# Performance work log

Measured on AMD Instinct MI355X. Metric: run time of the kernel, lower is better.

## Reference

```python
import jax, jax.numpy as jnp
from jax import lax
import numpy as np

C = 256; NH = 8; NP = 4; FFN = 512; B = 2; H = 128; W = 128
HD = C // NH


def _ln(x, g, b):
    m = jnp.mean(x, -1, keepdims=True)
    v = jnp.var(x, -1, keepdims=True)
    return (x - m) * lax.rsqrt(v + 1e-5) * g + b


def _deform_attn(q, kv, off_w, off_b, attw_w, attw_b, vp_w, vp_b, op_w, op_b):
    # q, kv: (B, N, C) with N = H*W
    Bn, N, Cc = q.shape
    val = (kv @ vp_w + vp_b).reshape(Bn, N, NH, HD)
    off = (q @ off_w + off_b).reshape(Bn, N, NH, NP, 2)
    attw = jax.nn.softmax((q @ attw_w + attw_b).reshape(Bn, N, NH, NP), axis=-1)
    # identity-grid reference points (normalized, pixel centers)
    ry = (jnp.arange(H, dtype=q.dtype) + 0.5) / H
    rx = (jnp.arange(W, dtype=q.dtype) + 0.5) / W
    gy, gx = jnp.meshgrid(ry, rx, indexing='ij')
    ref = jnp.stack([gx.ravel(), gy.ravel()], -1)  # (N, 2) as (x, y)
    norm = jnp.array([W, H], dtype=q.dtype)
    loc = ref[None, :, None, None, :] + off / norm  # (B,N,NH,NP,2) in [0,1]
    # grid_sample align_corners=False, zeros padding
    x = loc[..., 0] * W - 0.5
    y = loc[..., 1] * H - 0.5
    x0 = jnp.floor(x); y0 = jnp.floor(y)
    lx = x - x0; ly = y - y0
    x0i = x0.astype(jnp.int32); y0i = y0.astype(jnp.int32)
    v_t = val.transpose(0, 2, 1, 3)  # (B, NH, N, HD)

    def gather(xi, yi, w):
        valid = (xi >= 0) & (xi < W) & (yi >= 0) & (yi < H)
        idx = jnp.clip(yi, 0, H - 1) * W + jnp.clip(xi, 0, W - 1)  # (B,N,NH,NP)
        idx_t = idx.transpose(0, 2, 1, 3).reshape(Bn, NH, N * NP)
        g = jnp.take_along_axis(v_t, idx_t[..., None], axis=2)
        g = g.reshape(Bn, NH, N, NP, HD)
        wm = (w * valid).transpose(0, 2, 1, 3)  # (B,NH,N,NP)
        return g * wm[..., None]

    samp = (gather(x0i, y0i, (1 - lx) * (1 - ly))
            + gather(x0i + 1, y0i, lx * (1 - ly))
            + gather(x0i, y0i + 1, (1 - lx) * ly)
            + gather(x0i + 1, y0i + 1, lx * ly))  # (B,NH,N,NP,HD)
    out = jnp.einsum('bhnpd,bnhp->bnhd', samp, attw).reshape(Bn, N, Cc)
    return out @ op_w + op_b


def _forward(cam_bev, sat_bev,
             c2s_off_w, c2s_off_b, c2s_attw_w, c2s_attw_b, c2s_vp_w, c2s_vp_b, c2s_op_w, c2s_op_b,
             s2c_off_w, s2c_off_b, s2c_attw_w, s2c_attw_b, s2c_vp_w, s2c_vp_b, s2c_op_w, s2c_op_b,
             ln1_g, ln1_b, ln2_g, ln2_b, lnf_g, lnf_b,
             ffn1_w, ffn1_b, ffn2_w, ffn2_b,
             g1_w, bn_g, bn_b, g2_w, g2_b):
    Bn, Cc, Hh, Ww = cam_bev.shape
    q_cam = cam_bev.reshape(Bn, Cc, Hh * Ww).transpose(0, 2, 1)
    q_sat = sat_bev.reshape(Bn, Cc, Hh * Ww).transpose(0, 2, 1)
    c2s = _deform_attn(q_cam, q_sat, c2s_off_w, c2s_off_b, c2s_attw_w, c2s_attw_b,
                       c2s_vp_w, c2s_vp_b, c2s_op_w, c2s_op_b)
    cam_att = _ln(q_cam + c2s, ln1_g, ln1_b)
    s2c = _deform_attn(q_sat, q_cam, s2c_off_w, s2c_off_b, s2c_attw_w, s2c_attw_b,
                       s2c_vp_w, s2c_vp_b, s2c_op_w, s2c_op_b)
    sat_att = _ln(q_sat + s2c, ln2_g, ln2_b)
    cam_map = cam_att.transpose(0, 2, 1).reshape(Bn, Cc, Hh, Ww)
    sat_map = sat_att.transpose(0, 2, 1).reshape(Bn, Cc, Hh, Ww)
    gi = jnp.concatenate([cam_map, sat_map], axis=1)
    h = lax.conv_general_dilated(gi, g1_w, (1, 1), 'SAME',
                                 dimension_numbers=('NCHW', 'OIHW', 'NCHW'))
    # BatchNorm2d in eval mode: running_mean=0, running_var=1
    h = jax.nn.relu(h * lax.rsqrt(jnp.float32(1.0 + 1e-5)) * bn_g[None, :, None, None]
                    + bn_b[None, :, None, None])
    g = jax.nn.sigmoid(jnp.einsum('bchw,oc->bohw', h, g2_w) + g2_b[None, :, None, None])
    fused = g * cam_map + (1 - g) * sat_map
    ff = fused.reshape(Bn, Cc, Hh * Ww).transpose(0, 2, 1)
    ff = ff + (jax.nn.relu(ff @ ffn1_w + ffn1_b) @ ffn2_w + ffn2_b)
    ff = _ln(ff, lnf_g, lnf_b)
    return ff.transpose(0, 2, 1).reshape(Bn, Cc, Hh, Ww) + cam_bev


def setup_inputs() -> dict:
    key = jax.random.key(0)
    ks = iter(jax.random.split(key, 40))

    def rn(shape, s=0.02):
        return jax.random.normal(next(ks), shape, jnp.float32) * s

    # directional offset-bias init (as in original init_weights)
    thetas = np.arange(NH) * (2.0 * np.pi / NH)
    grid = np.stack([np.cos(thetas), np.sin(thetas)], -1)
    grid = grid / np.abs(grid).max(-1, keepdims=True)
    grid = np.tile(grid[:, None, :], (1, NP, 1)) * np.arange(1, NP + 1)[None, :, None]
    off_bias = jnp.asarray(grid.reshape(-1), jnp.float32)

    def attn_params():
        return dict(off_w=rn((C, NH * NP * 2), 0.01), off_b=off_bias,
                    attw_w=rn((C, NH * NP), 0.02), attw_b=rn((NH * NP,), 0.02),
                    vp_w=rn((C, C), 0.05), vp_b=jnp.zeros((C,), jnp.float32),
                    op_w=rn((C, C), 0.05), op_b=jnp.zeros((C,), jnp.float32))

    p1 = attn_params(); p2 = attn_params()
    inp = {
        'cam_bev': jax.random.normal(next(ks), (B, C, H, W), jnp.float32),
        'sat_bev': jax.random.normal(next(ks), (B, C, H, W), jnp.float32),
    }
    for pre, p in (('c2s_', p1), ('s2c_', p2)):
        for k, v in p.items():
            inp[pre + k] = v
    inp.update(
        ln1_g=jnp.ones((C,), jnp.float32), ln1_b=jnp.zeros((C,), jnp.float32),
        ln2_g=jnp.ones((C,), jnp.float32), ln2_b=jnp.zeros((C,), jnp.float32),
        lnf_g=jnp.ones((C,), jnp.float32), lnf_b=jnp.zeros((C,), jnp.float32),
        ffn1_w=rn((C, FFN), 0.05), ffn1_b=jnp.zeros((FFN,), jnp.float32),
        ffn2_w=rn((FFN, C), 0.05), ffn2_b=jnp.zeros((C,), jnp.float32),
        g1_w=rn((C // 2, 2 * C, 3, 3), 0.02),
        bn_g=jnp.ones((C // 2,), jnp.float32), bn_b=jnp.zeros((C // 2,), jnp.float32),
        g2_w=rn((C, C // 2), 0.02), g2_b=jnp.zeros((C,), jnp.float32),
    )
    return inp


def reference(cam_bev, sat_bev,
              c2s_off_w, c2s_off_b, c2s_attw_w, c2s_attw_b, c2s_vp_w, c2s_vp_b, c2s_op_w, c2s_op_b,
              s2c_off_w, s2c_off_b, s2c_attw_w, s2c_attw_b, s2c_vp_w, s2c_vp_b, s2c_op_w, s2c_op_b,
              ln1_g, ln1_b, ln2_g, ln2_b, lnf_g, lnf_b,
              ffn1_w, ffn1_b, ffn2_w, ffn2_b,
              g1_w, bn_g, bn_b, g2_w, g2_b):
    return _forward(cam_bev, sat_bev,
                    c2s_off_w, c2s_off_b, c2s_attw_w, c2s_attw_b, c2s_vp_w, c2s_vp_b, c2s_op_w, c2s_op_b,
                    s2c_off_w, s2c_off_b, s2c_attw_w, s2c_attw_b, s2c_vp_w, s2c_vp_b, s2c_op_w, s2c_op_b,
                    ln1_g, ln1_b, ln2_g, ln2_b, lnf_g, lnf_b,
                    ffn1_w, ffn1_b, ffn2_w, ffn2_b,
                    g1_w, bn_g, bn_b, g2_w, g2_b)
```

## Files before the change

### kernel.cpp

```cpp
#include <hip/hip_runtime.h>
#include <hip/hip_bf16.h>
#include <cstddef>

#define BBn  2
#define CCn  256
#define HHn  128
#define WWn  128
#define NNn  (HHn*WWn)
#define MTOT (BBn*NNn)
#define PADW 130

typedef unsigned short u16;
typedef __attribute__((ext_vector_type(8))) short bf8v;
typedef __attribute__((ext_vector_type(8))) unsigned short u16x8;
typedef __attribute__((ext_vector_type(4))) float f4v;

typedef __attribute__((address_space(1))) const void gvoid_t;
typedef __attribute__((address_space(3))) void svoid_t;
#define ASYNC16(g, l) __builtin_amdgcn_global_load_lds((gvoid_t*)(g), (svoid_t*)(l), 16, 0, 0)

__device__ __forceinline__ u16 f2bf(float f) {
    __hip_bfloat16 h = __float2bfloat16(f);
    return *reinterpret_cast<u16*>(&h);
}
__device__ __forceinline__ float bf2f(u16 h) {
    return __uint_as_float(((unsigned)h) << 16);
}

struct ZOff {
    long a, w, bia, f1, f2, b1, r, p;
    int ch;
};

template<int BM, int BN, int WC, int EPI, int KK>
__global__ __launch_bounds__(256)
void mgemm(const u16* __restrict__ A, const u16* __restrict__ Wt,
           const float* __restrict__ bias, int ldw, int Nc,
           float* __restrict__ outf, float* __restrict__ outf2,
           u16* __restrict__ outb, const u16* __restrict__ img,
           const void* __restrict__ resid,
           const float* __restrict__ p0, const float* __restrict__ p1,
           int choff, ZOff zo)
{
    constexpr int WR = 4 / WC;
    constexpr int MROWS = BM / WR;
    constexpr int MI = MROWS / 16;
    constexpr int AT = BM / 64;
    constexpr int BT = BN / 64;
    constexpr int NSTEPS = KK / 32;

    __shared__ __align__(16) u16 As[2 * BM * 32];
    __shared__ __align__(16) u16 Bs[2 * BN * 32];
    __shared__ float red[4][64][2];

    const int z = blockIdx.z;
    if (z) {
        A += (long)z * zo.a; Wt += (long)z * zo.w;
        if (bias)  bias  += (long)z * zo.bia;
        if (outf)  outf  += (long)z * zo.f1;
        if (outf2) outf2 += (long)z * zo.f2;
        if (outb)  outb  += (long)z * zo.b1;
        if (p0)    p0    += (long)z * zo.p;
        if (p1)    p1    += (long)z * zo.p;
        choff += z * zo.ch;
    }

    const int tid  = threadIdx.x;
    const int lane = tid & 63;
    const int w    = tid >> 6;
    const int wr   = w / WC, wc = w % WC;
    const int by = blockIdx.y;
    const int m0 = by * BM;
    const int n0 = blockIdx.x * BN;
    const int lr = lane & 15, lq = lane >> 4;

    const u16* gA[AT]; int loA[AT];
    #pragma unroll
    for (int t = 0; t < AT; ++t) {
        int c = t * 256 + tid; int row = c >> 2; int part = c & 3;
        int pg = part ^ ((row >> 1) & 3);
        gA[t] = A + (size_t)(m0 + row) * KK + pg * 8;
        loA[t] = c * 8;
    }
    const u16* gB[BT]; int loB[BT];
    #pragma unroll
    for (int t = 0; t < BT; ++t) {
        int c = t * 256 + tid; int row = c >> 2; int part = c & 3;
        int pg = part ^ ((row >> 1) & 3);
        gB[t] = Wt + (size_t)(n0 + row) * ldw + pg * 8;
        loB[t] = c * 8;
    }

    f4v acc[MI][4];
    if constexpr (EPI == 7 || EPI == 9) {
        const u16* r16 = (const u16*)resid + (EPI == 7 ? (long)z * zo.r : 0);
        #pragma unroll
        for (int j = 0; j < 4; ++j) {
            int n = wc * 64 + j * 16 + lr;
            float bj = bias[n];
            #pragma unroll
            for (int i = 0; i < MI; ++i)
                #pragma unroll
                for (int r = 0; r < 4; ++r) {
                    int m = m0 + i * 16 + lq * 4 + r;
                    acc[i][j][r] = bf2f(r16[(size_t)m * 256 + n]) + bj;
                }
        }
    } else {
        #pragma unroll
        for (int i = 0; i < MI; ++i)
            #pragma unroll
            for (int j = 0; j < 4; ++j)
                acc[i][j] = (f4v){0.f, 0.f, 0.f, 0.f};
    }

    auto stageG = [&](int s, int buf) {
        int k0 = s * 32;
        #pragma unroll
        for (int t = 0; t < AT; ++t)
            ASYNC16(gA[t] + k0, (u16*)As + buf * (BM * 32) + loA[t]);
        #pragma unroll
        for (int t = 0; t < BT; ++t)
            ASYNC16(gB[t] + k0, (u16*)Bs + buf * (BN * 32) + loB[t]);
    };
    auto computeStep = [&](int s) {
        const u16* Ab = As + (s & 1) * (BM * 32);
        const u16* Bb = Bs + (s & 1) * (BN * 32);
        bf8v af[MI], bv[4];
        #pragma unroll
        for (int i = 0; i < MI; ++i) {
            int row = wr * MROWS + i * 16 + lr;
            af[i] = *(const bf8v*)&Ab[row * 32 + ((lq ^ ((row >> 1) & 3)) << 3)];
        }
        #pragma unroll
        for (int j = 0; j < 4; ++j) {
            int row = wc * 64 + j * 16 + lr;
            bv[j] = *(const bf8v*)&Bb[row * 32 + ((lq ^ ((row >> 1) & 3)) << 3)];
        }
        #pragma unroll
        for (int i = 0; i < MI; ++i)
            #pragma unroll
            for (int j = 0; j < 4; ++j)
                acc[i][j] = __builtin_amdgcn_mfma_f32_16x16x32_bf16(af[i], bv[j], acc[i][j], 0, 0, 0);
    };

    stageG(0, 0);
    __syncthreads();
    for (int s = 0; s < NSTEPS - 1; ++s) {
        stageG(s + 1, (s + 1) & 1);
        computeStep(s);
        __syncthreads();
    }
    computeStep(NSTEPS - 1);

    if constexpr (EPI == 7 || EPI == 9) {
        float g4[4], b4[4];
        #pragma unroll
        for (int j = 0; j < 4; ++j) {
            int n = wc * 64 + j * 16 + lr;
            g4[j] = p0[n]; b4[j] = p1[n];
        }
        #pragma unroll
        for (int i = 0; i < MI; ++i)
            #pragma unroll
            for (int r = 0; r < 4; ++r) {
                float p = 0.f, p2 = 0.f;
                #pragma unroll
                for (int j = 0; j < 4; ++j) { float v = acc[i][j][r]; p += v; p2 += v * v; }
                p += __shfl_xor(p, 1, 16);  p2 += __shfl_xor(p2, 1, 16);
                p += __shfl_xor(p, 2, 16);  p2 += __shfl_xor(p2, 2, 16);
                p += __shfl_xor(p, 4, 16);  p2 += __shfl_xor(p2, 4, 16);
                p += __shfl_xor(p, 8, 16);  p2 += __shfl_xor(p2, 8, 16);
                if (lr == 0) {
                    int row = i * 16 + lq * 4 + r;
                    red[w][row][0] = p; red[w][row][1] = p2;
                }
            }
        __syncthreads();
        #pragma unroll
        for (int i = 0; i < MI; ++i) {
            float mean4[4], rstd4[4];
            #pragma unroll
            for (int r = 0; r < 4; ++r) {
                int row = i * 16 + lq * 4 + r;
                float s  = red[0][row][0] + red[1][row][0] + red[2][row][0] + red[3][row][0];
                float s2 = red[0][row][1] + red[1][row][1] + red[2][row][1] + red[3][row][1];
                float mean = s * (1.f / 256.f);
                float var  = s2 * (1.f / 256.f) - mean * mean;
                mean4[r] = mean;
                rstd4[r] = rsqrtf(var + 1e-5f);
            }
            if constexpr (EPI == 7) {
                #pragma unroll
                for (int r = 0; r < 4; ++r) {
                    int m = m0 + i * 16 + lq * 4 + r;
                    int b = m >> 14, sp = m & (NNn - 1);
                    size_t pb = (((size_t)b * PADW + (sp >> 7) + 1) * PADW + (sp & 127) + 1) * 512 + choff;
                    #pragma unroll
                    for (int j = 0; j < 4; ++j) {
                        int n = wc * 64 + j * 16 + lr;
                        outb[pb + n] = f2bf((acc[i][j][r] - mean4[r]) * rstd4[r] * g4[j] + b4[j]);
                    }
                }
            } else {
                int mb = m0 + i * 16 + lq * 4;
                int b = mb >> 14, sp = mb & (NNn - 1);
                #pragma unroll
                for (int j = 0; j < 4; ++j) {
                    int n = wc * 64 + j * 16 + lr;
                    size_t oi = ((size_t)b * 256 + n) * NNn + sp;
                    float4 cv = *(const float4*)&outf2[oi];
                    float4 o;
                    o.x = (acc[i][j][0] - mean4[0]) * rstd4[0] * g4[j] + b4[j] + cv.x;
                    o.y = (acc[i][j][1] - mean4[1]) * rstd4[1] * g4[j] + b4[j] + cv.y;
                    o.z = (acc[i][j][2] - mean4[2]) * rstd4[2] * g4[j] + b4[j] + cv.z;
                    o.w = (acc[i][j][3] - mean4[3]) * rstd4[3] * g4[j] + b4[j] + cv.w;
                    *(float4*)&outf[oi] = o;
                }
            }
        }
        return;
    }

    float bj[4]; int ncol[4];
    #pragma unroll
    for (int j = 0; j < 4; ++j) {
        int n = n0 + wc * 64 + j * 16 + lr;
        ncol[j] = n;
        if constexpr (EPI == 0 || EPI == 4 || EPI == 5) bj[j] = bias[n];
    }
    #pragma unroll
    for (int i = 0; i < MI; ++i) {
        #pragma unroll
        for (int r = 0; r < 4; ++r) {
            int m = m0 + wr * MROWS + i * 16 + lq * 4 + r;
            size_t pb = 0;
            if constexpr (EPI == 4) {
                int b = m >> 14, sp = m & (NNn - 1);
                pb = (((size_t)b * PADW + (sp >> 7) + 1) * PADW + (sp & 127) + 1) * 512;
            }
            #pragma unroll
            for (int j = 0; j < 4; ++j) {
                int n = ncol[j];
                float v = acc[i][j][r];
                size_t oi = (size_t)m * Nc + n;
                if constexpr (EPI == 0) {
                    outb[oi] = f2bf(v + bj[j]);
                } else if constexpr (EPI == 2) {
                    if (n < 64)      outf [(size_t)m * 64 + n]        = v + p0[n];
                    else if (n < 96) outf2[(size_t)m * 32 + (n - 64)] = v + p1[n - 64];
                } else if constexpr (EPI == 4) {
                    float vv = v + bj[j];
                    float g = 1.f / (1.f + __expf(-vv));
                    float f = g * bf2f(img[pb + n]) + (1.f - g) * bf2f(img[pb + 256 + n]);
                    outb[oi] = f2bf(f);
                } else if constexpr (EPI == 5) {
                    outb[oi] = f2bf(fmaxf(v + bj[j], 0.f));
                }
            }
        }
    }
}

template<int TAPS>
__global__ __launch_bounds__(256)
void conv_k(const u16* __restrict__ img, const u16* __restrict__ Wt,
            u16* __restrict__ outp)
{
    constexpr int NS = TAPS * 16;
    __shared__ __align__(16) u16 As[2 * 128 * 32];
    __shared__ __align__(16) u16 Bs[2 * 128 * 32];

    const int z = blockIdx.z;
    outp += (size_t)z * MTOT * 128;
    const int tid = threadIdx.x;
    const int lane = tid & 63;
    const int w = tid >> 6;
    const int wr = w >> 1, wc = w & 1;
    int by = blockIdx.y;
    by = ((by & 7) << 5) | (by >> 3);
    const int m0 = by * 128;
    const int lr = lane & 15, lq = lane >> 4;

    const u16* abase[2]; const u16* bbase[2]; int ldsOff[2];
    #pragma unroll
    for (int t = 0; t < 2; ++t) {
        int c = t * 256 + tid;
        int row = c >> 2, part = c & 3;
        int pg = part ^ ((row >> 1) & 3);
        ldsOff[t] = c * 8;
        int m = m0 + row; int b = m >> 14; int sp = m & (NNn - 1);
        long cb = ((long)b * PADW + (sp >> 7)) * PADW + (sp & 127);
        abase[t] = img + cb * 512 + pg * 8;
        bbase[t] = Wt + (size_t)row * 4608 + pg * 8;
    }

    long adel[TAPS]; int bdel[TAPS];
    #pragma unroll
    for (int tt = 0; tt < TAPS; ++tt) {
        int tap = z * TAPS + tt;
        int dy = tap / 3, dx = tap - dy * 3;
        adel[tt] = (long)(dy * PADW + dx) * 512;
        bdel[tt] = tap * 512;
    }

    f4v acc[4][4];
    #pragma unroll
    for (int i = 0; i < 4; ++i)
        #pragma unroll
        for (int j = 0; j < 4; ++j)
            acc[i][j] = (f4v){0.f, 0.f, 0.f, 0.f};

    auto stage = [&](int s, int buf) {
        int tt = s >> 4;
        int ci = (s & 15) * 32;
        #pragma unroll
        for (int t = 0; t < 2; ++t) {
            ASYNC16(abase[t] + adel[tt] + ci, (u16*)As + buf * (128 * 32) + ldsOff[t]);
            ASYNC16(bbase[t] + bdel[tt] + ci, (u16*)Bs + buf * (128 * 32) + ldsOff[t]);
        }
    };
    auto computeStep = [&](int s) {
        const u16* Ab = As + (s & 1) * (128 * 32);
        const u16* Bb = Bs + (s & 1) * (128 * 32);
        bf8v af[4], bv[4];
        #pragma unroll
        for (int i = 0; i < 4; ++i) {
            int row = wr * 64 + i * 16 + lr;
            af[i] = *(const bf8v*)&Ab[row * 32 + ((lq ^ ((row >> 1) & 3)) << 3)];
        }
        #pragma unroll
        for (int j = 0; j < 4; ++j) {
            int row = wc * 64 + j * 16 + lr;
            bv[j] = *(const bf8v*)&Bb[row * 32 + ((lq ^ ((row >> 1) & 3)) << 3)];
        }
        #pragma unroll
        for (int i = 0; i < 4; ++i)
            #pragma unroll
            for (int j = 0; j < 4; ++j)
                acc[i][j] = __builtin_amdgcn_mfma_f32_16x16x32_bf16(af[i], bv[j], acc[i][j], 0, 0, 0);
    };

    stage(0, 0);
    __syncthreads();
    #pragma unroll 4
    for (int s = 0; s < NS - 1; ++s) {
        stage(s + 1, (s + 1) & 1);
        computeStep(s);
        __syncthreads();
    }
    computeStep(NS - 1);

    #pragma unroll
    for (int i = 0; i < 4; ++i)
        #pragma unroll
        for (int r = 0; r < 4; ++r) {
            int m = m0 + wr * 64 + i * 16 + lq * 4 + r;
            #pragma unroll
            for (int j = 0; j < 4; ++j) {
                int n = wc * 64 + j * 16 + lr;
                outp[(size_t)m * 128 + n] = f2bf(acc[i][j][r]);
            }
        }
}

__global__ __launch_bounds__(256)
void combine_k(const u16* __restrict__ part, const float* __restrict__ bng,
               const float* __restrict__ bnb, u16* __restrict__ hb)
{
    const float bnscale = rsqrtf(1.0f + 1e-5f);
    int i = (blockIdx.x * 256 + threadIdx.x) * 4;
    int n = i & 127;
    float s0 = 0.f, s1 = 0.f, s2 = 0.f, s3 = 0.f;
    #pragma unroll
    for (int p = 0; p < 3; ++p) {
        ushort4 a = *(const ushort4*)&part[(size_t)p * MTOT * 128 + i];
        s0 += bf2f(a.x); s1 += bf2f(a.y); s2 += bf2f(a.z); s3 += bf2f(a.w);
    }
    ushort4 o;
    o.x = f2bf(fmaxf(s0 * bnscale * bng[n + 0] + bnb[n + 0], 0.f));
    o.y = f2bf(fmaxf(s1 * bnscale * bng[n + 1] + bnb[n + 1], 0.f));
    o.z = f2bf(fmaxf(s2 * bnscale * bng[n + 2] + bnb[n + 2], 0.f));
    o.w = f2bf(fmaxf(s3 * bnscale * bng[n + 3] + bnb[n + 3], 0.f));
    *(ushort4*)&hb[i] = o;
}

__global__ __launch_bounds__(256)
void zring_k(u16* __restrict__ pad)
{
    int i = blockIdx.x * 256 + threadIdx.x;
    if (i >= 66048) return;
    int e = i * 8;
    const int per_b = 264192;
    int b = e / per_b; int r = e - b * per_b;
    long off;
    if (r < 66560)       { int x = r >> 9, c = r & 511;                 off = (((long)b * PADW + 0)   * PADW + x)   * 512 + c; }
    else if (r < 133120) { int r2 = r - 66560;  int x = r2 >> 9, c = r2 & 511; off = (((long)b * PADW + 129) * PADW + x)   * 512 + c; }
    else if (r < 198656) { int r2 = r - 133120; int y = (r2 >> 9) + 1, c = r2 & 511; off = (((long)b * PADW + y)   * PADW + 0)   * 512 + c; }
    else                 { int r2 = r - 198656; int y = (r2 >> 9) + 1, c = r2 & 511; off = (((long)b * PADW + y)   * PADW + 129) * 512 + c; }
    *(u16x8*)(pad + off) = (u16x8){0, 0, 0, 0, 0, 0, 0, 0};
}

__global__ __launch_bounds__(256)
void tcvt_k(const float* __restrict__ cam, const float* __restrict__ sat,
            u16* __restrict__ qcam, u16* __restrict__ qsat)
{
    __shared__ float t[64][65];
    int z = blockIdx.z;
    const float* src = (z < 2) ? cam : sat;
    u16* dst = (z < 2) ? qcam : qsat;
    int b = z & 1;
    int c0 = blockIdx.x * 64, sp0 = blockIdx.y * 64;
    #pragma unroll
    for (int it = 0; it < 16; ++it) {
        int idx = it * 256 + threadIdx.x;
        int cl = idx >> 6, sl = idx & 63;
        t[cl][sl] = src[((size_t)(b * CCn + c0 + cl)) * NNn + sp0 + sl];
    }
    __syncthreads();
    #pragma unroll
    for (int it = 0; it < 16; ++it) {
        int idx = it * 256 + threadIdx.x;
        int sl = idx >> 6, cl = idx & 63;
        dst[((size_t)(b * NNn + sp0 + sl)) * CCn + c0 + cl] = f2bf(t[cl][sl]);
    }
}

__global__ __launch_bounds__(256)
void sample_k(const u16* __restrict__ val, const float* __restrict__ off,
              const float* __restrict__ lg, u16* __restrict__ outp)
{
    __shared__ uint2 desc[64][17];

    int z = blockIdx.z;
    val  += (size_t)z * MTOT * CCn;
    off  += (size_t)z * MTOT * 64;
    lg   += (size_t)z * MTOT * 32;
    outp += (size_t)z * MTOT * CCn;

    const int tid = threadIdx.x;
    const int rh0 = blockIdx.x * 64;

    if (tid < 64) {
        int rhg = rh0 + tid;
        int h = rhg & 7, rn = rhg >> 3;
        int n = rn & (NNn - 1), b = rn >> 14;
        int yp = n >> 7, xp = n & 127;

        const float* ofp = off + (size_t)rn * 64 + h * 8;
        const float* lgp = lg  + (size_t)rn * 32 + h * 4;
        float4 of0 = *(const float4*)ofp;
        float4 of1 = *(const float4*)(ofp + 4);
        float4 lgv = *(const float4*)lgp;
        float ofx[4] = { of0.x, of0.z, of1.x, of1.z };
        float ofy[4] = { of0.y, of0.w, of1.y, of1.w };

        float mx = fmaxf(fmaxf(lgv.x, lgv.y), fmaxf(lgv.z, lgv.w));
        float e0 = __expf(lgv.x - mx), e1 = __expf(lgv.y - mx);
        float e2 = __expf(lgv.z - mx), e3 = __expf(lgv.w - mx);
        float inv = 1.f / (e0 + e1 + e2 + e3);
        float aw[4] = { e0 * inv, e1 * inv, e2 * inv, e3 * inv };

        unsigned hb = (unsigned)(b * NNn) * 256u + h * 32;
        #pragma unroll
        for (int p = 0; p < 4; ++p) {
            float xs = (float)xp + ofx[p];
            float ys = (float)yp + ofy[p];
            float x0f = floorf(xs), y0f = floorf(ys);
            float lx = xs - x0f, ly = ys - y0f;
            int x0 = (int)x0f, y0 = (int)y0f;
            #pragma unroll
            for (int c = 0; c < 4; ++c) {
                int xi = x0 + (c & 1), yi = y0 + (c >> 1);
                bool valid = (xi >= 0) & (xi < WWn) & (yi >= 0) & (yi < HHn);
                float wgt = valid
                    ? aw[p] * ((c & 1) ? lx : 1.f - lx) * ((c >> 1) ? ly : 1.f - ly)
                    : 0.f;
                int xc = min(max(xi, 0), WWn - 1);
                int yc = min(max(yi, 0), HHn - 1);
                unsigned addr = hb + (unsigned)(yc * WWn + xc) * 256u;
                desc[tid][p * 4 + c] = make_uint2(addr, __float_as_uint(wgt));
            }
        }
    }
    __syncthreads();

    const int rh = tid >> 2;
    const int q  = tid & 3;
    const int rhg = rh0 + rh;
    const int h = rhg & 7, rn = rhg >> 3;

    float a[8];
    #pragma unroll
    for (int e = 0; e < 8; ++e) a[e] = 0.f;
    #pragma unroll
    for (int k = 0; k < 16; ++k) {
        uint2 d = desc[rh][k];
        float wgt = __uint_as_float(d.y);
        u16x8 v = *(const u16x8*)(val + d.x + q * 8);
        #pragma unroll
        for (int e = 0; e < 8; ++e)
            a[e] += wgt * bf2f(v[e]);
    }
    u16x8 o;
    #pragma unroll
    for (int e = 0; e < 8; ++e) o[e] = f2bf(a[e]);
    *(u16x8*)(outp + (size_t)rn * CCn + h * 32 + q * 8) = o;
}

__global__ __launch_bounds__(256)
void repack_all(const float* __restrict__ vp1, const float* __restrict__ op1,
                const float* __restrict__ vp2, const float* __restrict__ op2,
                const float* __restrict__ f1w, const float* __restrict__ f2w,
                const float* __restrict__ of1, const float* __restrict__ aw1,
                const float* __restrict__ of2, const float* __restrict__ aw2,
                const float* __restrict__ g1,  const float* __restrict__ g2,
                const float* __restrict__ vpb1, const float* __restrict__ vpb2,
                const float* __restrict__ opb1, const float* __restrict__ opb2,
                const float* __restrict__ ofb1, const float* __restrict__ awb1,
                const float* __restrict__ ofb2, const float* __restrict__ awb2,
                const float* __restrict__ l1g, const float* __restrict__ l1b,
                const float* __restrict__ l2g, const float* __restrict__ l2b,
                u16* __restrict__ wb, float* __restrict__ bb)
{
    int i = blockIdx.x * 256 + threadIdx.x;
    if (i >= 1212416 + 2240) return;
    if (i >= 1212416) {
        int j = i - 1212416;
        float v;
        if      (j < 256)  v = vpb1[j];
        else if (j < 512)  v = vpb2[j - 256];
        else if (j < 768)  v = opb1[j - 512];
        else if (j < 1024) v = opb2[j - 768];
        else if (j < 1088) v = ofb1[j - 1024];
        else if (j < 1120) v = awb1[j - 1088];
        else if (j < 1184) v = ofb2[j - 1120];
        else if (j < 1216) v = awb2[j - 1184];
        else if (j < 1472) v = l1g[j - 1216];
        else if (j < 1728) v = l1b[j - 1472];
        else if (j < 1984) v = l2g[j - 1728];
        else               v = l2b[j - 1984];
        bb[j] = v;
        return;
    }
    float v;
    if (i < 262144) {
        const float* src[4] = { vp1, vp2, op1, op2 };
        int q = i >> 16, j = i & 65535;
        int n = j >> 8, k = j & 255;
        v = src[q][(size_t)k * 256 + n];
    } else if (i < 393216) {
        int j = i - 262144; int n = j >> 8, k = j & 255;
        v = f1w[(size_t)k * 512 + n];
    } else if (i < 524288) {
        int j = i - 393216; int n = j >> 9, k = j & 511;
        v = f2w[(size_t)k * 256 + n];
    } else if (i < 589824) {
        int jj = i - 524288; int hh = jj >> 15; int j = jj & 32767;
        int n = j >> 8, k = j & 255;
        const float* ofw = hh ? of2 : of1;
        const float* aww = hh ? aw2 : aw1;
        if (n < 64)      v = ofw[(size_t)k * 64 + n];
        else if (n < 96) v = aww[(size_t)k * 32 + (n - 64)];
        else             v = 0.f;
    } else if (i < 1179648) {
        int j = i - 589824; int co = j / 4608, k = j - co * 4608;
        int tap = k >> 9, ci = k & 511;
        v = g1[((size_t)co * 512 + ci) * 9 + tap];
    } else {
        int j = i - 1179648; int n = j >> 7, k = j & 127;
        v = g2[(size_t)n * 128 + k];
    }
    wb[i] = f2bf(v);
}

extern "C" void kernel_launch(void* const* d_in, const int* in_sizes, int n_in,
                              void* d_out, int out_size, void* d_ws, size_t ws_size,
                              hipStream_t stream)
{
    const float* cam_bev   = (const float*)d_in[0];
    const float* sat_bev   = (const float*)d_in[1];
    const float* c2s_off_w  = (const float*)d_in[2];
    const float* c2s_off_b  = (const float*)d_in[3];
    const float* c2s_attw_w = (const float*)d_in[4];
    const float* c2s_attw_b = (const float*)d_in[5];
    const float* c2s_vp_w   = (const float*)d_in[6];
    const float* c2s_vp_b   = (const float*)d_in[7];
    const float* c2s_op_w   = (const float*)d_in[8];
    const float* c2s_op_b   = (const float*)d_in[9];
    const float* s2c_off_w  = (const float*)d_in[10];
    const float* s2c_off_b  = (const float*)d_in[11];
    const float* s2c_attw_w = (const float*)d_in[12];
    const float* s2c_attw_b = (const float*)d_in[13];
    const float* s2c_vp_w   = (const float*)d_in[14];
    const float* s2c_vp_b   = (const float*)d_in[15];
    const float* s2c_op_w   = (const float*)d_in[16];
    const float* s2c_op_b   = (const float*)d_in[17];
    const float* ln1_g = (const float*)d_in[18];
    const float* ln1_b = (const float*)d_in[19];
    const float* ln2_g = (const float*)d_in[20];
    const float* ln2_b = (const float*)d_in[21];
    const float* lnf_g = (const float*)d_in[22];
    const float* lnf_b = (const float*)d_in[23];
    const float* ffn1_w = (const float*)d_in[24];
    const float* ffn1_b = (const float*)d_in[25];
    const float* ffn2_w = (const float*)d_in[26];
    const float* ffn2_b = (const float*)d_in[27];
    const float* g1_w  = (const float*)d_in[28];
    const float* bn_g  = (const float*)d_in[29];
    const float* bn_b  = (const float*)d_in[30];
    const float* g2_w  = (const float*)d_in[31];
    const float* g2_b  = (const float*)d_in[32];

    char* base = (char*)d_ws;
    size_t off = 0;
    auto alloc = [&](size_t bytes) -> void* {
        void* p = base + off;
        off += (bytes + 255) & ~(size_t)255;
        return p;
    };

    u16*   qcam   = (u16*)  alloc((size_t)MTOT * CCn * 2 * 2);
    u16*   qsat   = qcam + (size_t)MTOT * CCn;
    u16*   valb   = (u16*)  alloc((size_t)MTOT * CCn * 2 * 2);
    u16*   sampb  = (u16*)  alloc((size_t)MTOT * CCn * 2 * 2);
    float* offb   = (float*)alloc((size_t)MTOT * 64 * 4 * 2);
    float* attwb  = (float*)alloc((size_t)MTOT * 32 * 4 * 2);
    size_t padBytes = (size_t)BBn * PADW * PADW * 512 * 2;
    u16*   pad    = (u16*)  alloc(padBytes);
    u16*   hbuf   = (u16*)  alloc((size_t)MTOT * 128 * 2);
    u16*   convpart = (u16*)alloc((size_t)3 * MTOT * 128 * 2);
    u16*   wbase  = (u16*)  alloc((size_t)1212416 * 2);
    float* biasbf = (float*)alloc((size_t)2240 * 4);
    u16* wvp = wbase;
    u16* wop = wbase + 131072;
    u16* wf1 = wbase + 262144;
    u16* wf2 = wbase + 393216;
    u16* woa = wbase + 524288;
    u16* wcv = wbase + 589824;
    u16* wg2 = wbase + 1179648;
    u16*   fused_bf = valb;
    u16*   midb     = qcam;

    dim3 blk(256);
    ZOff zz{0, 0, 0, 0, 0, 0, 0, 0, 0};

    zring_k<<<258, blk, 0, stream>>>(pad);
    tcvt_k<<<dim3(4, 256, 4), blk, 0, stream>>>(cam_bev, sat_bev, qcam, qsat);
    repack_all<<<4746, blk, 0, stream>>>(c2s_vp_w, c2s_op_w, s2c_vp_w, s2c_op_w,
                                         ffn1_w, ffn2_w, c2s_off_w, c2s_attw_w,
                                         s2c_off_w, s2c_attw_w, g1_w, g2_w,
                                         c2s_vp_b, s2c_vp_b, c2s_op_b, s2c_op_b,
                                         c2s_off_b, c2s_attw_b, s2c_off_b, s2c_attw_b,
                                         ln1_g, ln1_b, ln2_g, ln2_b,
                                         wbase, biasbf);

    {
        ZOff zo{ -(long)MTOT * CCn, 65536, 256, 0, 0, (long)MTOT * CCn, 0, 0, 0 };
        mgemm<128, 128, 2, 0, 256><<<dim3(2, 256, 2), blk, 0, stream>>>(
            qsat, wvp, biasbf, 256, 256,
            nullptr, nullptr, valb, nullptr, nullptr, nullptr, nullptr, 0, zo);
    }
    {
        ZOff zo{ (long)MTOT * CCn, 32768, 0, (long)MTOT * 64, (long)MTOT * 32, 0, 0, 96, 0 };
        mgemm<64, 128, 2, 2, 256><<<dim3(1, 512, 2), blk, 0, stream>>>(
            qcam, woa, nullptr, 256, 128,
            offb, attwb, nullptr, nullptr, nullptr, biasbf + 1024, biasbf + 1088, 0, zo);
    }
    sample_k<<<dim3(4096, 1, 2), blk, 0, stream>>>(valb, offb, attwb, sampb);
    {
        ZOff zo{ (long)MTOT * CCn, 65536, 256, 0, 0, 0, (long)MTOT * CCn, 512, 256 };
        mgemm<64, 256, 4, 7, 256><<<dim3(1, 512, 2), blk, 0, stream>>>(
            sampb, wop, biasbf + 512, 256, 256,
            nullptr, nullptr, pad, nullptr, qcam, biasbf + 1216, biasbf + 1472, 0, zo);
    }
    conv_k<3><<<dim3(1, 256, 3), blk, 0, stream>>>(pad, wcv, convpart);
    combine_k<<<4096, blk, 0, stream>>>(convpart, bn_g, bn_b, hbuf);

    mgemm<64, 128, 2, 4, 128><<<dim3(2, 512, 1), blk, 0, stream>>>(
        hbuf, wg2, g2_b, 128, 256,
        nullptr, nullptr, fused_bf, pad, nullptr, nullptr, nullptr, 0, zz);

    mgemm<128, 128, 2, 5, 256><<<dim3(4, 256, 1), blk, 0, stream>>>(
        fused_bf, wf1, ffn1_b, 256, 512,
        nullptr, nullptr, midb, nullptr, nullptr, nullptr, nullptr, 0, zz);
    mgemm<64, 256, 4, 9, 512><<<dim3(1, 512, 1), blk, 0, stream>>>(
        midb, wf2, ffn2_b, 512, 256,
        (float*)d_out, (float*)cam_bev, nullptr, nullptr, fused_bf, lnf_g, lnf_b, 0, zz);
}
```

Before: 279.7 us.

## Merge prologue kernels and fuse value-proj with offset/attn GEMM into one launch

Combines the ring-zeroing, input transpose/convert and weight repack kernels into a single prologue launch, and merges the value-projection GEMM and the offset/attention-logit GEMM into one kernel that dispatches blocks by job. The aim is to cut launch count and the tail bubbles between small dependent kernels, letting the two independent GEMMs share the GPU concurrently. The combined GEMM computes all 128 columns for the offset job, where the old config used a narrower tile. Block-level branching may also lower occupancy uniformity.

```diff
diff --git a/kernel.cpp b/kernel.cpp
--- a/kernel.cpp
+++ b/kernel.cpp
@@ -227,7 +227,7 @@
     for (int j = 0; j < 4; ++j) {
         int n = n0 + wc * 64 + j * 16 + lr;
         ncol[j] = n;
-        if constexpr (EPI == 0 || EPI == 4 || EPI == 5) bj[j] = bias[n];
+        if constexpr (EPI == 4 || EPI == 5) bj[j] = bias[n];
     }
     #pragma unroll
     for (int i = 0; i < MI; ++i) {
@@ -244,12 +244,7 @@
                 int n = ncol[j];
                 float v = acc[i][j][r];
                 size_t oi = (size_t)m * Nc + n;
-                if constexpr (EPI == 0) {
-                    outb[oi] = f2bf(v + bj[j]);
-                } else if constexpr (EPI == 2) {
-                    if (n < 64)      outf [(size_t)m * 64 + n]        = v + p0[n];
-                    else if (n < 96) outf2[(size_t)m * 32 + (n - 64)] = v + p1[n - 64];
-                } else if constexpr (EPI == 4) {
+                if constexpr (EPI == 4) {
                     float vv = v + bj[j];
                     float g = 1.f / (1.f + __expf(-vv));
                     float f = g * bf2f(img[pb + n]) + (1.f - g) * bf2f(img[pb + 256 + n]);
@@ -259,6 +254,126 @@
                 }
             }
         }
+    }
+}
+
+__global__ __launch_bounds__(256)
+void vpoa_k(const u16* __restrict__ qcam, const u16* __restrict__ wvp,
+            const u16* __restrict__ woa, const float* __restrict__ biasbf,
+            u16* __restrict__ valb, float* __restrict__ offb,
+            float* __restrict__ attwb)
+{
+    __shared__ __align__(16) u16 As[2 * 128 * 32];
+    __shared__ __align__(16) u16 Bs[2 * 128 * 32];
+
+    const int bx = blockIdx.x;
+    int job, zs, by, n0;
+    if (bx < 1024) { job = 0; zs = bx >> 9; int r = bx & 511; n0 = (r & 1) * 128; by = r >> 1; }
+    else           { job = 1; int r = bx - 1024; zs = r >> 8; by = r & 255; n0 = 0; }
+
+    const u16* A  = job == 0 ? qcam + (size_t)(1 - zs) * MTOT * CCn
+                             : qcam + (size_t)zs * MTOT * CCn;
+    const u16* Wt = job == 0 ? wvp + zs * 65536 : woa + zs * 32768;
+
+    const int tid  = threadIdx.x;
+    const int lane = tid & 63;
+    const int w    = tid >> 6;
+    const int wr   = w >> 1, wc = w & 1;
+    const int m0 = by * 128;
+    const int lr = lane & 15, lq = lane >> 4;
+
+    const u16* gA[2]; int loA[2];
+    const u16* gB[2]; int loB[2];
+    #pragma unroll
+    for (int t = 0; t < 2; ++t) {
+        int c = t * 256 + tid; int row = c >> 2; int part = c & 3;
+        int pg = part ^ ((row >> 1) & 3);
+        gA[t] = A + (size_t)(m0 + row) * 256 + pg * 8;
+        gB[t] = Wt + (size_t)(n0 + row) * 256 + pg * 8;
+        loA[t] = c * 8; loB[t] = c * 8;
+    }
+
+    f4v acc[4][4];
+    #pragma unroll
+    for (int i = 0; i < 4; ++i)
+        #pragma unroll
+        for (int j = 0; j < 4; ++j)
+            acc[i][j] = (f4v){0.f, 0.f, 0.f, 0.f};
+
+    auto stageG = [&](int s, int buf) {
+        int k0 = s * 32;
+        #pragma unroll
+        for (int t = 0; t < 2; ++t) {
+            ASYNC16(gA[t] + k0, (u16*)As + buf * (128 * 32) + loA[t]);
+            ASYNC16(gB[t] + k0, (u16*)Bs + buf * (128 * 32) + loB[t]);
+        }
+    };
+    auto computeStep = [&](int s) {
+        const u16* Ab = As + (s & 1) * (128 * 32);
+        const u16* Bb = Bs + (s & 1) * (128 * 32);
+        bf8v af[4], bv[4];
+        #pragma unroll
+        for (int i = 0; i < 4; ++i) {
+            int row = wr * 64 + i * 16 + lr;
+            af[i] = *(const bf8v*)&Ab[row * 32 + ((lq ^ ((row >> 1) & 3)) << 3)];
+        }
+        #pragma unroll
+        for (int j = 0; j < 4; ++j) {
+            int row = wc * 64 + j * 16 + lr;
+            bv[j] = *(const bf8v*)&Bb[row * 32 + ((lq ^ ((row >> 1) & 3)) << 3)];
+        }
+        #pragma unroll
+        for (int i = 0; i < 4; ++i)
+            #pragma unroll
+            for (int j = 0; j < 4; ++j)
+                acc[i][j] = __builtin_amdgcn_mfma_f32_16x16x32_bf16(af[i], bv[j], acc[i][j], 0, 0, 0);
+    };
+
+    stageG(0, 0);
+    __syncthreads();
+    for (int s = 0; s < 7; ++s) {
+        stageG(s + 1, (s + 1) & 1);
+        computeStep(s);
+        __syncthreads();
+    }
+    computeStep(7);
+
+    if (job == 0) {
+        u16* outb = valb + (size_t)zs * MTOT * CCn;
+        const float* bias = biasbf + zs * 256;
+        float bj[4]; int ncol[4];
+        #pragma unroll
+        for (int j = 0; j < 4; ++j) {
+            int n = n0 + wc * 64 + j * 16 + lr;
+            ncol[j] = n; bj[j] = bias[n];
+        }
+        #pragma unroll
+        for (int i = 0; i < 4; ++i)
+            #pragma unroll
+            for (int r = 0; r < 4; ++r) {
+                int m = m0 + wr * 64 + i * 16 + lq * 4 + r;
+                #pragma unroll
+                for (int j = 0; j < 4; ++j)
+                    outb[(size_t)m * 256 + ncol[j]] = f2bf(acc[i][j][r] + bj[j]);
+            }
+    } else {
+        float* of = offb + (size_t)zs * MTOT * 64;
+        float* aw = attwb + (size_t)zs * MTOT * 32;
+        const float* p0 = biasbf + 1024 + zs * 96;
+        const float* p1 = biasbf + 1088 + zs * 96;
+        #pragma unroll
+        for (int i = 0; i < 4; ++i)
+            #pragma unroll
+            for (int r = 0; r < 4; ++r) {
+                int m = m0 + wr * 64 + i * 16 + lq * 4 + r;
+                #pragma unroll
+                for (int j = 0; j < 4; ++j) {
+                    int n = wc * 64 + j * 16 + lr;
+                    float v = acc[i][j][r];
+                    if (n < 64)      of[(size_t)m * 64 + n]        = v + p0[n];
+                    else if (n < 96) aw[(size_t)m * 32 + (n - 64)] = v + p1[n - 64];
+                }
+            }
     }
 }
 
@@ -386,130 +501,9 @@
 }
 
 __global__ __launch_bounds__(256)
-void zring_k(u16* __restrict__ pad)
-{
-    int i = blockIdx.x * 256 + threadIdx.x;
-    if (i >= 66048) return;
-    int e = i * 8;
-    const int per_b = 264192;
-    int b = e / per_b; int r = e - b * per_b;
-    long off;
-    if (r < 66560)       { int x = r >> 9, c = r & 511;                 off = (((long)b * PADW + 0)   * PADW + x)   * 512 + c; }
-    else if (r < 133120) { int r2 = r - 66560;  int x = r2 >> 9, c = r2 & 511; off = (((long)b * PADW + 129) * PADW + x)   * 512 + c; }
-    else if (r < 198656) { int r2 = r - 133120; int y = (r2 >> 9) + 1, c = r2 & 511; off = (((long)b * PADW + y)   * PADW + 0)   * 512 + c; }
-    else                 { int r2 = r - 198656; int y = (r2 >> 9) + 1, c = r2 & 511; off = (((long)b * PADW + y)   * PADW + 129) * 512 + c; }
-    *(u16x8*)(pad + off) = (u16x8){0, 0, 0, 0, 0, 0, 0, 0};
-}
-
-__global__ __launch_bounds__(256)
-void tcvt_k(const float* __restrict__ cam, const float* __restrict__ sat,
-            u16* __restrict__ qcam, u16* __restrict__ qsat)
-{
-    __shared__ float t[64][65];
-    int z = blockIdx.z;
-    const float* src = (z < 2) ? cam : sat;
-    u16* dst = (z < 2) ? qcam : qsat;
-    int b = z & 1;
-    int c0 = blockIdx.x * 64, sp0 = blockIdx.y * 64;
-    #pragma unroll
-    for (int it = 0; it < 16; ++it) {
-        int idx = it * 256 + threadIdx.x;
-        int cl = idx >> 6, sl = idx & 63;
-        t[cl][sl] = src[((size_t)(b * CCn + c0 + cl)) * NNn + sp0 + sl];
-    }
-    __syncthreads();
-    #pragma unroll
-    for (int it = 0; it < 16; ++it) {
-        int idx = it * 256 + threadIdx.x;
-        int sl = idx >> 6, cl = idx & 63;
-        dst[((size_t)(b * NNn + sp0 + sl)) * CCn + c0 + cl] = f2bf(t[cl][sl]);
-    }
-}
-
-__global__ __launch_bounds__(256)
-void sample_k(const u16* __restrict__ val, const float* __restrict__ off,
-              const float* __restrict__ lg, u16* __restrict__ outp)
-{
-    __shared__ uint2 desc[64][17];
-
-    int z = blockIdx.z;
-    val  += (size_t)z * MTOT * CCn;
-    off  += (size_t)z * MTOT * 64;
-    lg   += (size_t)z * MTOT * 32;
-    outp += (size_t)z * MTOT * CCn;
-
-    const int tid = threadIdx.x;
-    const int rh0 = blockIdx.x * 64;
-
-    if (tid < 64) {
-        int rhg = rh0 + tid;
-        int h = rhg & 7, rn = rhg >> 3;
-        int n = rn & (NNn - 1), b = rn >> 14;
-        int yp = n >> 7, xp = n & 127;
-
-        const float* ofp = off + (size_t)rn * 64 + h * 8;
-        const float* lgp = lg  + (size_t)rn * 32 + h * 4;
-        float4 of0 = *(const float4*)ofp;
-        float4 of1 = *(const float4*)(ofp + 4);
-        float4 lgv = *(const float4*)lgp;
-        float ofx[4] = { of0.x, of0.z, of1.x, of1.z };
-        float ofy[4] = { of0.y, of0.w, of1.y, of1.w };
-
-        float mx = fmaxf(fmaxf(lgv.x, lgv.y), fmaxf(lgv.z, lgv.w));
-        float e0 = __expf(lgv.x - mx), e1 = __expf(lgv.y - mx);
-        float e2 = __expf(lgv.z - mx), e3 = __expf(lgv.w - mx);
-        float inv = 1.f / (e0 + e1 + e2 + e3);
-        float aw[4] = { e0 * inv, e1 * inv, e2 * inv, e3 * inv };
-
-        unsigned hb = (unsigned)(b * NNn) * 256u + h * 32;
-        #pragma unroll
-        for (int p = 0; p < 4; ++p) {
-            float xs = (float)xp + ofx[p];
-            float ys = (float)yp + ofy[p];
-            float x0f = floorf(xs), y0f = floorf(ys);
-            float lx = xs - x0f, ly = ys - y0f;
-            int x0 = (int)x0f, y0 = (int)y0f;
-            #pragma unroll
-            for (int c = 0; c < 4; ++c) {
-                int xi = x0 + (c & 1), yi = y0 + (c >> 1);
-                bool valid = (xi >= 0) & (xi < WWn) & (yi >= 0) & (yi < HHn);
-                float wgt = valid
-                    ? aw[p] * ((c & 1) ? lx : 1.f - lx) * ((c >> 1) ? ly : 1.f - ly)
-                    : 0.f;
-                int xc = min(max(xi, 0), WWn - 1);
-                int yc = min(max(yi, 0), HHn - 1);
-                unsigned addr = hb + (unsigned)(yc * WWn + xc) * 256u;
-                desc[tid][p * 4 + c] = make_uint2(addr, __float_as_uint(wgt));
-            }
-        }
-    }
-    __syncthreads();
-
-    const int rh = tid >> 2;
-    const int q  = tid & 3;
-    const int rhg = rh0 + rh;
-    const int h = rhg & 7, rn = rhg >> 3;
-
-    float a[8];
-    #pragma unroll
-    for (int e = 0; e < 8; ++e) a[e] = 0.f;
-    #pragma unroll
-    for (int k = 0; k < 16; ++k) {
-        uint2 d = desc[rh][k];
-        float wgt = __uint_as_float(d.y);
-        u16x8 v = *(const u16x8*)(val + d.x + q * 8);
-        #pragma unroll
-        for (int e = 0; e < 8; ++e)
-            a[e] += wgt * bf2f(v[e]);
-    }
-    u16x8 o;
-    #pragma unroll
-    for (int e = 0; e < 8; ++e) o[e] = f2bf(a[e]);
-    *(u16x8*)(outp + (size_t)rn * CCn + h * 32 + q * 8) = o;
-}
-
-__global__ __launch_bounds__(256)
-void repack_all(const float* __restrict__ vp1, const float* __restrict__ op1,
+void prologue_k(const float* __restrict__ cam, const float* __restrict__ sat,
+                u16* __restrict__ qcam, u16* __restrict__ qsat,
+                const float* __restrict__ vp1, const float* __restrict__ op1,
                 const float* __restrict__ vp2, const float* __restrict__ op2,
                 const float* __restrict__ f1w, const float* __restrict__ f2w,
                 const float* __restrict__ of1, const float* __restrict__ aw1,
@@ -521,57 +515,181 @@
                 const float* __restrict__ ofb2, const float* __restrict__ awb2,
                 const float* __restrict__ l1g, const float* __restrict__ l1b,
                 const float* __restrict__ l2g, const float* __restrict__ l2b,
-                u16* __restrict__ wb, float* __restrict__ bb)
+                u16* __restrict__ wb, float* __restrict__ bb,
+                u16* __restrict__ pad)
 {
-    int i = blockIdx.x * 256 + threadIdx.x;
-    if (i >= 1212416 + 2240) return;
-    if (i >= 1212416) {
-        int j = i - 1212416;
+    __shared__ float t[64][65];
+    const int bx = blockIdx.x;
+    const int tid = threadIdx.x;
+
+    if (bx < 4096) {
+        int x = bx & 3, y = (bx >> 2) & 255, zz = bx >> 10;
+        const float* src = (zz < 2) ? cam : sat;
+        u16* dst = (zz < 2) ? qcam : qsat;
+        int b = zz & 1;
+        int c0 = x * 64, sp0 = y * 64;
+        #pragma unroll
+        for (int it = 0; it < 16; ++it) {
+            int idx = it * 256 + tid;
+            int cl = idx >> 6, sl = idx & 63;
+            t[cl][sl] = src[((size_t)(b * CCn + c0 + cl)) * NNn + sp0 + sl];
+        }
+        __syncthreads();
+        #pragma unroll
+        for (int it = 0; it < 16; ++it) {
+            int idx = it * 256 + tid;
+            int sl = idx >> 6, cl = idx & 63;
+            dst[((size_t)(b * NNn + sp0 + sl)) * CCn + c0 + cl] = f2bf(t[cl][sl]);
+        }
+        return;
+    }
+    if (bx < 8842) {
+        int i = (bx - 4096) * 256 + tid;
+        if (i >= 1212416 + 2240) return;
+        if (i >= 1212416) {
+            int j = i - 1212416;
+            float v;
+            if      (j < 256)  v = vpb1[j];
+            else if (j < 512)  v = vpb2[j - 256];
+            else if (j < 768)  v = opb1[j - 512];
+            else if (j < 1024) v = opb2[j - 768];
+            else if (j < 1088) v = ofb1[j - 1024];
+            else if (j < 1120) v = awb1[j - 1088];
+            else if (j < 1184) v = ofb2[j - 1120];
+            else if (j < 1216) v = awb2[j - 1184];
+            else if (j < 1472) v = l1g[j - 1216];
+            else if (j < 1728) v = l1b[j - 1472];
+            else if (j < 1984) v = l2g[j - 1728];
+            else               v = l2b[j - 1984];
+            bb[j] = v;
+            return;
+        }
         float v;
-        if      (j < 256)  v = vpb1[j];
-        else if (j < 512)  v = vpb2[j - 256];
-        else if (j < 768)  v = opb1[j - 512];
-        else if (j < 1024) v = opb2[j - 768];
-        else if (j < 1088) v = ofb1[j - 1024];
-        else if (j < 1120) v = awb1[j - 1088];
-        else if (j < 1184) v = ofb2[j - 1120];
-        else if (j < 1216) v = awb2[j - 1184];
-        else if (j < 1472) v = l1g[j - 1216];
-        else if (j < 1728) v = l1b[j - 1472];
-        else if (j < 1984) v = l2g[j - 1728];
-        else               v = l2b[j - 1984];
-        bb[j] = v;
+        if (i < 262144) {
+            const float* src[4] = { vp1, vp2, op1, op2 };
+            int q = i >> 16, j = i & 65535;
+            int n = j >> 8, k = j & 255;
+            v = src[q][(size_t)k * 256 + n];
+        } else if (i < 393216) {
+            int j = i - 262144; int n = j >> 8, k = j & 255;
+            v = f1w[(size_t)k * 512 + n];
+        } else if (i < 524288) {
+            int j = i - 393216; int n = j >> 9, k = j & 511;
+            v = f2w[(size_t)k * 256 + n];
+        } else if (i < 589824) {
+            int jj = i - 524288; int hh = jj >> 15; int j = jj & 32767;
+            int n = j >> 8, k = j & 255;
+            const float* ofw = hh ? of2 : of1;
+            const float* aww = hh ? aw2 : aw1;
+            if (n < 64)      v = ofw[(size_t)k * 64 + n];
+            else if (n < 96) v = aww[(size_t)k * 32 + (n - 64)];
+            else             v = 0.f;
+        } else if (i < 1179648) {
+            int j = i - 589824; int co = j / 4608, k = j - co * 4608;
+            int tap = k >> 9, ci = k & 511;
+            v = g1[((size_t)co * 512 + ci) * 9 + tap];
+        } else {
+            int j = i - 1179648; int n = j >> 7, k = j & 127;
+            v = g2[(size_t)n * 128 + k];
+        }
+        wb[i] = f2bf(v);
         return;
     }
-    float v;
-    if (i < 262144) {
-        const float* src[4] = { vp1, vp2, op1, op2 };
-        int q = i >> 16, j = i & 65535;
-        int n = j >> 8, k = j & 255;
-        v = src[q][(size_t)k * 256 + n];
-    } else if (i < 393216) {
-        int j = i - 262144; int n = j >> 8, k = j & 255;
-        v = f1w[(size_t)k * 512 + n];
-    } else if (i < 524288) {
-        int j = i - 393216; int n = j >> 9, k = j & 511;
-        v = f2w[(size_t)k * 256 + n];
-    } else if (i < 589824) {
-        int jj = i - 524288; int hh = jj >> 15; int j = jj & 32767;
-        int n = j >> 8, k = j & 255;
-        const float* ofw = hh ? of2 : of1;
-        const float* aww = hh ? aw2 : aw1;
-        if (n < 64)      v = ofw[(size_t)k * 64 + n];
-        else if (n < 96) v = aww[(size_t)k * 32 + (n - 64)];
-        else             v = 0.f;
-    } else if (i < 1179648) {
-        int j = i - 589824; int co = j / 4608, k = j - co * 4608;
-        int tap = k >> 9, ci = k & 511;
-        v = g1[((size_t)co * 512 + ci) * 9 + tap];
-    } else {
-        int j = i - 1179648; int n = j >> 7, k = j & 127;
-        v = g2[(size_t)n * 128 + k];
-    }
-    wb[i] = f2bf(v);
+    {
+        int i = (bx - 8842) * 256 + tid;
+        if (i >= 66048) return;
+        int e = i * 8;
+        const int per_b = 264192;
+        int b = e / per_b; int r = e - b * per_b;
+        long off;
+        if (r < 66560)       { int x = r >> 9, c = r & 511;                 off = (((long)b * PADW + 0)   * PADW + x)   * 512 + c; }
+        else if (r < 133120) { int r2 = r - 66560;  int x = r2 >> 9, c = r2 & 511; off = (((long)b * PADW + 129) * PADW + x)   * 512 + c; }
+        else if (r < 198656) { int r2 = r - 133120; int y = (r2 >> 9) + 1, c = r2 & 511; off = (((long)b * PADW + y)   * PADW + 0)   * 512 + c; }
+        else                 { int r2 = r - 198656; int y = (r2 >> 9) + 1, c = r2 & 511; off = (((long)b * PADW + y)   * PADW + 129) * 512 + c; }
+        *(u16x8*)(pad + off) = (u16x8){0, 0, 0, 0, 0, 0, 0, 0};
+    }
+}
+
+__global__ __launch_bounds__(256)
+void sample_k(const u16* __restrict__ val, const float* __restrict__ off,
+              const float* __restrict__ lg, u16* __restrict__ outp)
+{
+    __shared__ uint2 desc[64][17];
+
+    int z = blockIdx.z;
+    val  += (size_t)z * MTOT * CCn;
+    off  += (size_t)z * MTOT * 64;
+    lg   += (size_t)z * MTOT * 32;
+    outp += (size_t)z * MTOT * CCn;
+
+    const int tid = threadIdx.x;
+    const int rh0 = blockIdx.x * 64;
+
+    if (tid < 64) {
+        int rhg = rh0 + tid;
+        int h = rhg & 7, rn = rhg >> 3;
+        int n = rn & (NNn - 1), b = rn >> 14;
+        int yp = n >> 7, xp = n & 127;
+
+        const float* ofp = off + (size_t)rn * 64 + h * 8;
+        const float* lgp = lg  + (size_t)rn * 32 + h * 4;
+        float4 of0 = *(const float4*)ofp;
+        float4 of1 = *(const float4*)(ofp + 4);
+        float4 lgv = *(const float4*)lgp;
+        float ofx[4] = { of0.x, of0.z, of1.x, of1.z };
+        float ofy[4] = { of0.y, of0.w, of1.y, of1.w };
+
+        float mx = fmaxf(fmaxf(lgv.x, lgv.y), fmaxf(lgv.z, lgv.w));
+        float e0 = __expf(lgv.x - mx), e1 = __expf(lgv.y - mx);
+        float e2 = __expf(lgv.z - mx), e3 = __expf(lgv.w - mx);
+        float inv = 1.f / (e0 + e1 + e2 + e3);
+        float aw[4] = { e0 * inv, e1 * inv, e2 * inv, e3 * inv };
+
+        unsigned hb = (unsigned)(b * NNn) * 256u + h * 32;
+        #pragma unroll
+        for (int p = 0; p < 4; ++p) {
+            float xs = (float)xp + ofx[p];
+            float ys = (float)yp + ofy[p];
+            float x0f = floorf(xs), y0f = floorf(ys);
+            float lx = xs - x0f, ly = ys - y0f;
+            int x0 = (int)x0f, y0 = (int)y0f;
+            #pragma unroll
+            for (int c = 0; c < 4; ++c) {
+                int xi = x0 + (c & 1), yi = y0 + (c >> 1);
+                bool valid = (xi >= 0) & (xi < WWn) & (yi >= 0) & (yi < HHn);
+                float wgt = valid
+                    ? aw[p] * ((c & 1) ? lx : 1.f - lx) * ((c >> 1) ? ly : 1.f - ly)
+                    : 0.f;
+                int xc = min(max(xi, 0), WWn - 1);
+                int yc = min(max(yi, 0), HHn - 1);
+                unsigned addr = hb + (unsigned)(yc * WWn + xc) * 256u;
+                desc[tid][p * 4 + c] = make_uint2(addr, __float_as_uint(wgt));
+            }
+        }
+    }
+    __syncthreads();
+
+    const int rh = tid >> 2;
+    const int q  = tid & 3;
+    const int rhg = rh0 + rh;
+    const int h = rhg & 7, rn = rhg >> 3;
+
+    float a[8];
+    #pragma unroll
+    for (int e = 0; e < 8; ++e) a[e] = 0.f;
+    #pragma unroll
+    for (int k = 0; k < 16; ++k) {
+        uint2 d = desc[rh][k];
+        float wgt = __uint_as_float(d.y);
+        u16x8 v = *(const u16x8*)(val + d.x + q * 8);
+        #pragma unroll
+        for (int e = 0; e < 8; ++e)
+            a[e] += wgt * bf2f(v[e]);
+    }
+    u16x8 o;
+    #pragma unroll
+    for (int e = 0; e < 8; ++e) o[e] = f2bf(a[e]);
+    *(u16x8*)(outp + (size_t)rn * CCn + h * 32 + q * 8) = o;
 }
 
 extern "C" void kernel_launch(void* const* d_in, const int* in_sizes, int n_in,
@@ -645,28 +763,18 @@
     dim3 blk(256);
     ZOff zz{0, 0, 0, 0, 0, 0, 0, 0, 0};
 
-    zring_k<<<258, blk, 0, stream>>>(pad);
-    tcvt_k<<<dim3(4, 256, 4), blk, 0, stream>>>(cam_bev, sat_bev, qcam, qsat);
-    repack_all<<<4746, blk, 0, stream>>>(c2s_vp_w, c2s_op_w, s2c_vp_w, s2c_op_w,
-                                         ffn1_w, ffn2_w, c2s_off_w, c2s_attw_w,
-                                         s2c_off_w, s2c_attw_w, g1_w, g2_w,
-                                         c2s_vp_b, s2c_vp_b, c2s_op_b, s2c_op_b,
-                                         c2s_off_b, c2s_attw_b, s2c_off_b, s2c_attw_b,
-                                         ln1_g, ln1_b, ln2_g, ln2_b,
-                                         wbase, biasbf);
-
-    {
-        ZOff zo{ -(long)MTOT * CCn, 65536, 256, 0, 0, (long)MTOT * CCn, 0, 0, 0 };
-        mgemm<128, 128, 2, 0, 256><<<dim3(2, 256, 2), blk, 0, stream>>>(
-            qsat, wvp, biasbf, 256, 256,
-            nullptr, nullptr, valb, nullptr, nullptr, nullptr, nullptr, 0, zo);
-    }
-    {
-        ZOff zo{ (long)MTOT * CCn, 32768, 0, (long)MTOT * 64, (long)MTOT * 32, 0, 0, 96, 0 };
-        mgemm<64, 128, 2, 2, 256><<<dim3(1, 512, 2), blk, 0, stream>>>(
-            qcam, woa, nullptr, 256, 128,
-            offb, attwb, nullptr, nullptr, nullptr, biasbf + 1024, biasbf + 1088, 0, zo);
-    }
+    prologue_k<<<9100, blk, 0, stream>>>(
+        cam_bev, sat_bev, qcam, qsat,
+        c2s_vp_w, c2s_op_w, s2c_vp_w, s2c_op_w,
+        ffn1_w, ffn2_w, c2s_off_w, c2s_attw_w,
+        s2c_off_w, s2c_attw_w, g1_w, g2_w,
+        c2s_vp_b, s2c_vp_b, c2s_op_b, s2c_op_b,
+        c2s_off_b, c2s_attw_b, s2c_off_b, s2c_attw_b,
+        ln1_g, ln1_b, ln2_g, ln2_b,
+        wbase, biasbf, pad);
+
+    vpoa_k<<<1536, blk, 0, stream>>>(qcam, wvp, woa, biasbf, valb, offb, attwb);
+
     sample_k<<<dim3(4096, 1, 2), blk, 0, stream>>>(valb, offb, attwb, sampb);
     {
         ZOff zo{ (long)MTOT * CCn, 65536, 256, 0, 0, 0, (long)MTOT * CCn, 512, 256 };
```

Result: faster. 267.5 us (median of 3 runs) (-4.4%).
